# Kernel optimization log

Hardware: AMD Instinct MI355X
Metric: run time of the kernel (lower is better)

## Reference

```python
import jax, jax.numpy as jnp
from jax import lax
import numpy as np


def setup_inputs() -> dict:
    key = jax.random.key(0)
    k1, k2, k3, k4, k5 = jax.random.split(key, 5)
    bs, m, v, L, P = 2, 16, 16, 40320, 32
    preds = jax.random.normal(k1, (bs, m, v, L), dtype=jnp.float32)
    target = jax.random.normal(k2, (bs, v, L), dtype=jnp.float32)
    weights = jax.random.uniform(k3, (L,), dtype=jnp.float32)
    scale = jax.random.uniform(k4, (v,), dtype=jnp.float32)
    # binary-ish patch masks over grid points (float, as in the torch buffer)
    masks = (jax.random.uniform(k5, (P, L)) < 0.25).astype(jnp.float32)
    return {"preds": preds, "target": target, "weights": weights,
            "scale": scale, "masks": masks, "beta": 1}


def _energy_score(x, y, m, beta):
    # x: (bs, m, D) ensemble, y: (bs, D) observation
    diff = x - y[:, None, :]
    a = jnp.sqrt(jnp.sum(diff * diff, axis=-1))            # (bs, m)
    score_a = jnp.mean(jnp.sum(a ** beta, axis=-1)) / m
    # pairwise distances via Gram trick (cdist p=2)
    sq = jnp.sum(x * x, axis=-1)                            # (bs, m)
    g = jnp.einsum('bid,bjd->bij', x, x)                    # (bs, m, m)
    d2 = jnp.maximum(sq[:, :, None] + sq[:, None, :] - 2.0 * g, 0.0)
    pos = d2 > 0
    d = jnp.where(pos, jnp.sqrt(jnp.where(pos, d2, 1.0)), 0.0)
    score_b = jnp.mean(jnp.sum(d ** beta, axis=(1, 2))) / (2 * m * (m - 1))
    return score_a - score_b


def reference(preds, target, weights, scale, masks, beta):
    beta = float(beta)
    bs, m, v, L = preds.shape
    # buffer scaling as in forward()
    p = preds * scale[None, None, :, None] * weights        # (bs, m, v, L)
    t = target * scale[None, :, None] * weights             # (bs, v, L)

    def body(acc, mask):
        # rearrange 'bs m v latlon -> bs m (latlon v)'
        x = (p * mask).transpose(0, 1, 3, 2).reshape(bs, m, L * v)
        y = (t * mask).transpose(0, 2, 1).reshape(bs, L * v)
        return acc + _energy_score(x, y, m, beta), None

    total, _ = lax.scan(body, jnp.float32(0.0), masks)
    return total
```

## Files before the change

### kernel.cpp

```cpp
#include <hip/hip_runtime.h>
#include <math.h>

#define BS 2
#define M 16
#define V 16
#define NROWB 136
#define NROWS 272
#define PMASK 32
#define NPB 630
#define NE 8704
#define PBSTRIDE 8704
#define SPLIT 30
#define QPB 21

typedef __attribute__((ext_vector_type(8))) short bf16x8;
typedef __attribute__((ext_vector_type(4))) float f32x4;
typedef __attribute__((ext_vector_type(4))) unsigned int u32x4;

static __device__ __forceinline__ unsigned short f2bf(float x) {
    unsigned int u = __float_as_uint(x);
    unsigned int r = (u + 0x7FFFu + ((u >> 16) & 1u)) >> 16;
    return (unsigned short)r;
}

static __device__ __forceinline__ void k1_stage(
    const float* __restrict__ preds, float* __restrict__ dst,
    int b, int v0, int l0, int L, int lane, int wave)
{
#pragma unroll
    for (int n = 0; n < 2; ++n) {
        int r0 = wave * 8 + n * 4;
        int r = r0 + (lane >> 4);
        int grow = b * 256 + (r >> 1) * 16 + v0 + (r & 1);
        const float* g = preds + (size_t)grow * L + l0 + (lane & 15) * 4;
        __builtin_amdgcn_global_load_lds(
            (const __attribute__((address_space(1))) unsigned int*)g,
            (__attribute__((address_space(3))) unsigned int*)(dst + r0 * 64),
            16, 0, 0);
    }
}

template<int W>
static __device__ __forceinline__ void k1_chunk(
    const float* __restrict__ xsb,
    const float* __restrict__ targ,
    const float* __restrict__ scl,
    float wl,
    int v0, int lane, float* __restrict__ acc)
{
    const int base = (W == 0) ? 0 : 34 * W - 16;
    const int npair = (W == 0) ? 18 : 34;
    const int aoff = (W == 0) ? 16 : 0;

#pragma unroll
    for (int vc = 0; vc < 2; ++vc) {
        const int v = v0 + vc;
        float s = scl[v] * wl;
        float x[M];
#pragma unroll
        for (int i = 0; i < M; ++i)
            x[i] = xsb[(i * 2 + vc) * 64 + lane] * s;
        if (W == 0) {
            float y = targ[v] * s;
#pragma unroll
            for (int i = 0; i < M; ++i) {
                float d = x[i] - y;
                acc[i] = fmaf(d, d, acc[i]);
            }
        }
        int k = 0;
#pragma unroll
        for (int i = 0; i < M; ++i) {
#pragma unroll
            for (int j = i + 1; j < M; ++j) {
                if (k >= base && k < base + npair) {
                    float d = x[i] - x[j];
                    acc[aoff + k - base] = fmaf(d, d, acc[aoff + k - base]);
                }
                ++k;
            }
        }
    }
}

__global__ __launch_bounds__(256, 2)
void k1_fused(const float* __restrict__ preds, const float* __restrict__ target,
              const float* __restrict__ weights, const float* __restrict__ scale,
              const float* __restrict__ masks, float* __restrict__ partial,
              float* __restrict__ out, int L)
{
    __shared__ float xs[2][2048];
    __shared__ unsigned short sld[144 * 64];

    const int t = (int)threadIdx.x;
    const int lane = t & 63, wave = t >> 6;
    const int pb = (int)blockIdx.x;
    const int b  = (int)blockIdx.y;
    const int l0 = pb * 64;

    if (pb == 0 && b == 0 && t == 0) out[0] = 0.0f;

    ((unsigned int*)sld)[136 * 32 + t] = 0;

    k1_stage(preds, &xs[0][0], b, 0, l0, L, lane, wave);

    float scl[V];
#pragma unroll
    for (int v = 0; v < V; ++v) scl[v] = scale[v];
    float wl = weights[l0 + lane];
    float targ[V];
    if (wave == 0) {
#pragma unroll
        for (int v = 0; v < V; ++v)
            targ[v] = target[(size_t)(b * V + v) * L + l0 + lane];
    }

    float acc[34];
#pragma unroll
    for (int r = 0; r < 34; ++r) acc[r] = 0.0f;

#pragma unroll
    for (int s = 0; s < 8; ++s) {
        __syncthreads();
        if (s < 7)
            k1_stage(preds, &xs[(s + 1) & 1][0], b, (s + 1) * 2, l0, L, lane, wave);
        const float* xsb = &xs[s & 1][0];
        switch (wave) {
            case 0: k1_chunk<0>(xsb, targ, scl, wl, s * 2, lane, acc); break;
            case 1: k1_chunk<1>(xsb, targ, scl, wl, s * 2, lane, acc); break;
            case 2: k1_chunk<2>(xsb, targ, scl, wl, s * 2, lane, acc); break;
            default: k1_chunk<3>(xsb, targ, scl, wl, s * 2, lane, acc); break;
        }
    }

#pragma unroll
    for (int r = 0; r < 34; ++r) {
        const int R = 34 * wave + r;
        sld[R * 64 + (lane ^ ((R & 7) << 3))] = f2bf(acc[r]);
    }
    __syncthreads();

    const int ntile = (wave == 3) ? 3 : 2;
    f32x4 pacc[3][2];
#pragma unroll
    for (int ti = 0; ti < 3; ++ti)
#pragma unroll
        for (int pt = 0; pt < 2; ++pt)
            pacc[ti][pt] = (f32x4){0.f, 0.f, 0.f, 0.f};

#pragma unroll
    for (int ks = 0; ks < 2; ++ks) {
        bf16x8 bfr[2];
#pragma unroll
        for (int pt = 0; pt < 2; ++pt) {
            const float* mp = masks + (size_t)(pt * 16 + (lane & 15)) * L
                            + l0 + ks * 32 + (lane >> 4) * 8;
            u32x4 m0 = *(const u32x4*)mp;
            u32x4 m1 = *(const u32x4*)(mp + 4);
            union { unsigned int u[4]; bf16x8 v; } bb;
            bb.u[0] = __builtin_amdgcn_perm(m0.y, m0.x, 0x07060302);
            bb.u[1] = __builtin_amdgcn_perm(m0.w, m0.z, 0x07060302);
            bb.u[2] = __builtin_amdgcn_perm(m1.y, m1.x, 0x07060302);
            bb.u[3] = __builtin_amdgcn_perm(m1.w, m1.z, 0x07060302);
            bfr[pt] = bb.v;
        }
#pragma unroll
        for (int ti = 0; ti < 3; ++ti) {
            if (ti >= ntile) continue;
            const int tile = (ti == 2) ? 8 : (wave + ti * 4);
            const bf16x8 a = *(const bf16x8*)&sld[
                (tile * 16 + (lane & 15)) * 64 +
                ((ks * 32 + (lane >> 4) * 8) ^ ((lane & 7) << 3))];
            pacc[ti][0] = __builtin_amdgcn_mfma_f32_16x16x32_bf16(
                a, bfr[0], pacc[ti][0], 0, 0, 0);
            pacc[ti][1] = __builtin_amdgcn_mfma_f32_16x16x32_bf16(
                a, bfr[1], pacc[ti][1], 0, 0, 0);
        }
    }

    float* P = partial + (size_t)(pb * 2 + b) * (NROWB * PMASK);
#pragma unroll
    for (int ti = 0; ti < 3; ++ti) {
        if (ti >= ntile) continue;
        const int tile = (ti == 2) ? 8 : (wave + ti * 4);
#pragma unroll
        for (int pt = 0; pt < 2; ++pt)
#pragma unroll
            for (int reg = 0; reg < 4; ++reg) {
                const int row = tile * 16 + (lane >> 4) * 4 + reg;
                if (row < NROWB)
                    P[row * 32 + pt * 16 + (lane & 15)] = pacc[ti][pt][reg];
            }
    }
}

__global__ __launch_bounds__(256, 2)
void k3a_reduce(const float* __restrict__ P, float* __restrict__ P2)
{
    const int t = (int)threadIdx.x;
    const int e = (int)blockIdx.x * 256 + t;
    const int spl = (int)blockIdx.y;

    const float* p = P + (size_t)(spl * QPB) * PBSTRIDE + e;
    float a0 = 0.f, a1 = 0.f, a2 = 0.f;
#pragma unroll
    for (int q = 0; q < QPB; q += 3) {
        a0 += p[(size_t)(q    ) * PBSTRIDE];
        a1 += p[(size_t)(q + 1) * PBSTRIDE];
        a2 += p[(size_t)(q + 2) * PBSTRIDE];
    }
    P2[(size_t)spl * NE + e] = (a0 + a1) + a2;
}

__global__ __launch_bounds__(256, 2)
void k3b_finalize(const float* __restrict__ P2, const int* __restrict__ beta_p,
                  float* __restrict__ out)
{
    const int t = (int)threadIdx.x;
    const int e = (int)blockIdx.x * 256 + t;

    float a0 = 0.f, a1 = 0.f, a2 = 0.f;
#pragma unroll
    for (int q = 0; q < SPLIT; q += 3) {
        a0 += P2[(size_t)(q    ) * NE + e];
        a1 += P2[(size_t)(q + 1) * NE + e];
        a2 += P2[(size_t)(q + 2) * NE + e];
    }
    float d2 = fmaxf((a0 + a1) + a2, 0.0f);
    float beta = (float)beta_p[0];
    float d = (beta == 1.0f) ? sqrtf(d2) : powf(d2, 0.5f * beta);

    const float wa = 1.0f / (float)(BS * M);
    const float wb = -1.0f / (float)(BS * M * (M - 1));
    const int row_g = e >> 5;
    const int local = row_g % NROWB;
    float sum = ((local < M) ? wa : wb) * d;

    const int lane = t & 63, wv = t >> 6;
#pragma unroll
    for (int off = 32; off > 0; off >>= 1)
        sum += __shfl_down(sum, off, 64);
    __shared__ float red[4];
    if (lane == 0) red[wv] = sum;
    __syncthreads();
    if (t == 0)
        atomicAdd(out, red[0] + red[1] + red[2] + red[3]);
}

extern "C" void kernel_launch(void* const* d_in, const int* in_sizes, int n_in,
                              void* d_out, int out_size, void* d_ws, size_t ws_size,
                              hipStream_t stream)
{
    const float* preds   = (const float*)d_in[0];
    const float* target  = (const float*)d_in[1];
    const float* weights = (const float*)d_in[2];
    const float* scale   = (const float*)d_in[3];
    const float* masks   = (const float*)d_in[4];
    const int*   beta    = (const int*)d_in[5];
    float* out = (float*)d_out;

    int L = in_sizes[2];

    float* partial = (float*)d_ws;
    size_t p_bytes = (size_t)NPB * 2 * NROWB * PMASK * sizeof(float);
    float* partial2 = (float*)((char*)d_ws + ((p_bytes + 255) & ~(size_t)255));

    dim3 g1(NPB, BS);
    k1_fused<<<g1, 256, 0, stream>>>(preds, target, weights, scale, masks,
                                     partial, out, L);

    dim3 g3a(NE / 256, SPLIT);
    k3a_reduce<<<g3a, 256, 0, stream>>>(partial, partial2);

    k3b_finalize<<<NE / 256, 256, 0, stream>>>(partial2, beta, out);
}
```

Measured before the change: 152.5 us.

## Load preds directly to registers per wave, drop LDS staging and barriers

Replaces the shared-memory double-buffered staging of preds (global_load_lds plus __syncthreads per v-pair) with per-wave direct global loads into registers, software-pipelined one v ahead. Scale*weight products and scaled targets are precomputed once. This removes LDS traffic and block-wide barriers in the pairwise-distance phase. In exchange, each of the four waves now reads the full preds tile from global memory, four times the global/L2 traffic of the shared staging, and register pressure rises.

```diff
diff --git a/kernel.cpp b/kernel.cpp
--- a/kernel.cpp
+++ b/kernel.cpp
@@ -23,63 +23,66 @@
     return (unsigned short)r;
 }
 
-static __device__ __forceinline__ void k1_stage(
-    const float* __restrict__ preds, float* __restrict__ dst,
-    int b, int v0, int l0, int L, int lane, int wave)
-{
-#pragma unroll
-    for (int n = 0; n < 2; ++n) {
-        int r0 = wave * 8 + n * 4;
-        int r = r0 + (lane >> 4);
-        int grow = b * 256 + (r >> 1) * 16 + v0 + (r & 1);
-        const float* g = preds + (size_t)grow * L + l0 + (lane & 15) * 4;
-        __builtin_amdgcn_global_load_lds(
-            (const __attribute__((address_space(1))) unsigned int*)g,
-            (__attribute__((address_space(3))) unsigned int*)(dst + r0 * 64),
-            16, 0, 0);
-    }
-}
-
 template<int W>
-static __device__ __forceinline__ void k1_chunk(
-    const float* __restrict__ xsb,
-    const float* __restrict__ targ,
-    const float* __restrict__ scl,
-    float wl,
-    int v0, int lane, float* __restrict__ acc)
+static __device__ __forceinline__ void pairs_one(
+    const float* __restrict__ xr,
+    float s,
+    float y,
+    float* __restrict__ acc)
 {
     const int base = (W == 0) ? 0 : 34 * W - 16;
     const int npair = (W == 0) ? 18 : 34;
     const int aoff = (W == 0) ? 16 : 0;
 
-#pragma unroll
-    for (int vc = 0; vc < 2; ++vc) {
-        const int v = v0 + vc;
-        float s = scl[v] * wl;
-        float x[M];
+    float x[M];
+#pragma unroll
+    for (int i = 0; i < M; ++i) x[i] = xr[i] * s;
+    if (W == 0) {
+#pragma unroll
+        for (int i = 0; i < M; ++i) {
+            float d = x[i] - y;
+            acc[i] = fmaf(d, d, acc[i]);
+        }
+    }
+    int k = 0;
+#pragma unroll
+    for (int i = 0; i < M; ++i) {
+#pragma unroll
+        for (int j = i + 1; j < M; ++j) {
+            if (k >= base && k < base + npair) {
+                float d = x[i] - x[j];
+                acc[aoff + k - base] = fmaf(d, d, acc[aoff + k - base]);
+            }
+            ++k;
+        }
+    }
+}
+
+template<int W>
+static __device__ __forceinline__ void k1_body(
+    const float* __restrict__ pB,
+    size_t Ls,
+    const float* __restrict__ sw,
+    const float* __restrict__ ty,
+    float* __restrict__ acc)
+{
+    float xa[M], xb[M];
+#pragma unroll
+    for (int i = 0; i < M; ++i) xa[i] = pB[(size_t)(i * 16) * Ls];
+
+#pragma unroll
+    for (int h = 0; h < 8; ++h) {
+        const int v0 = 2 * h, v1 = 2 * h + 1;
 #pragma unroll
         for (int i = 0; i < M; ++i)
-            x[i] = xsb[(i * 2 + vc) * 64 + lane] * s;
-        if (W == 0) {
-            float y = targ[v] * s;
-#pragma unroll
-            for (int i = 0; i < M; ++i) {
-                float d = x[i] - y;
-                acc[i] = fmaf(d, d, acc[i]);
-            }
-        }
-        int k = 0;
-#pragma unroll
-        for (int i = 0; i < M; ++i) {
-#pragma unroll
-            for (int j = i + 1; j < M; ++j) {
-                if (k >= base && k < base + npair) {
-                    float d = x[i] - x[j];
-                    acc[aoff + k - base] = fmaf(d, d, acc[aoff + k - base]);
-                }
-                ++k;
-            }
-        }
+            xb[i] = pB[(size_t)(i * 16 + v1) * Ls];
+        pairs_one<W>(xa, sw[v0], (W == 0) ? ty[v0] : 0.0f, acc);
+        if (h < 7) {
+#pragma unroll
+            for (int i = 0; i < M; ++i)
+                xa[i] = pB[(size_t)(i * 16 + v1 + 1) * Ls];
+        }
+        pairs_one<W>(xb, sw[v1], (W == 0) ? ty[v1] : 0.0f, acc);
     }
 }
 
@@ -89,7 +92,6 @@
               const float* __restrict__ masks, float* __restrict__ partial,
               float* __restrict__ out, int L)
 {
-    __shared__ float xs[2][2048];
     __shared__ unsigned short sld[144 * 64];
 
     const int t = (int)threadIdx.x;
@@ -102,35 +104,29 @@
 
     ((unsigned int*)sld)[136 * 32 + t] = 0;
 
-    k1_stage(preds, &xs[0][0], b, 0, l0, L, lane, wave);
-
-    float scl[V];
-#pragma unroll
-    for (int v = 0; v < V; ++v) scl[v] = scale[v];
-    float wl = weights[l0 + lane];
-    float targ[V];
+    const size_t Ls = (size_t)L;
+    const float wl = weights[l0 + lane];
+    float sw[V];
+#pragma unroll
+    for (int v = 0; v < V; ++v) sw[v] = scale[v] * wl;
+    float ty[V];
     if (wave == 0) {
 #pragma unroll
         for (int v = 0; v < V; ++v)
-            targ[v] = target[(size_t)(b * V + v) * L + l0 + lane];
-    }
+            ty[v] = target[(size_t)(b * V + v) * Ls + l0 + lane] * sw[v];
+    }
+
+    const float* pB = preds + (size_t)b * 256 * Ls + l0 + lane;
 
     float acc[34];
 #pragma unroll
     for (int r = 0; r < 34; ++r) acc[r] = 0.0f;
 
-#pragma unroll
-    for (int s = 0; s < 8; ++s) {
-        __syncthreads();
-        if (s < 7)
-            k1_stage(preds, &xs[(s + 1) & 1][0], b, (s + 1) * 2, l0, L, lane, wave);
-        const float* xsb = &xs[s & 1][0];
-        switch (wave) {
-            case 0: k1_chunk<0>(xsb, targ, scl, wl, s * 2, lane, acc); break;
-            case 1: k1_chunk<1>(xsb, targ, scl, wl, s * 2, lane, acc); break;
-            case 2: k1_chunk<2>(xsb, targ, scl, wl, s * 2, lane, acc); break;
-            default: k1_chunk<3>(xsb, targ, scl, wl, s * 2, lane, acc); break;
-        }
+    switch (wave) {
+        case 0: k1_body<0>(pB, Ls, sw, ty, acc); break;
+        case 1: k1_body<1>(pB, Ls, sw, ty, acc); break;
+        case 2: k1_body<2>(pB, Ls, sw, ty, acc); break;
+        default: k1_body<3>(pB, Ls, sw, ty, acc); break;
     }
 
 #pragma unroll
@@ -153,7 +149,7 @@
         bf16x8 bfr[2];
 #pragma unroll
         for (int pt = 0; pt < 2; ++pt) {
-            const float* mp = masks + (size_t)(pt * 16 + (lane & 15)) * L
+            const float* mp = masks + (size_t)(pt * 16 + (lane & 15)) * Ls
                             + l0 + ks * 32 + (lane >> 4) * 8;
             u32x4 m0 = *(const u32x4*)mp;
             u32x4 m1 = *(const u32x4*)(mp + 4);
```

Result: slower. 203.6 us (+33.5%).
